# Kernel optimization log

Measured on AMD Instinct MI355X. Metric: run time of the kernel, lower is better.

Reference implementation:

```python
import jax, jax.numpy as jnp
import numpy as np

N_HEAD = 12
HEAD_SIZE = 64  # 768 / 12
SCALE = 1.0 / np.sqrt(HEAD_SIZE)


def setup_inputs() -> dict:
    key = jax.random.key(0)
    k1, k2, k3 = jax.random.split(key, 3)
    B, T, C = 8, 1024, 768
    x = jax.random.normal(k1, (B, T, C), dtype=jnp.float32)
    W_attn = jax.random.normal(k2, (C, 3 * C), dtype=jnp.float32) * 0.02
    b_attn = jax.random.normal(k3, (3 * C,), dtype=jnp.float32) * 0.02
    return {"x": x, "W_attn": W_attn, "b_attn": b_attn}


def reference(x, W_attn, b_attn):
    B, T, C = x.shape
    hs = C // N_HEAD
    qkv = x @ W_attn + b_attn                      # [B, T, 3C]
    q, k, v = jnp.split(qkv, 3, axis=-1)
    # [B, nh, T, hs]
    q = q.reshape(B, T, N_HEAD, hs).transpose(0, 2, 1, 3)
    k = k.reshape(B, T, N_HEAD, hs).transpose(0, 2, 1, 3)
    v = v.reshape(B, T, N_HEAD, hs).transpose(0, 2, 1, 3)
    scores = jnp.einsum('bhqd,bhkd->bhqk', q, k) * SCALE
    causal = jnp.tril(jnp.ones((T, T), dtype=bool))  # [T, T]
    # masked positions get -inf then relu -> 0; equivalent to where(mask, relu, 0)
    att = jnp.where(causal, jax.nn.relu(scores), 0.0)
    y = jnp.einsum('bhqk,bhkd->bhqd', att, v)      # [B, nh, T, hs]
    return y.transpose(0, 2, 1, 3).reshape(B, T, C)
```

## Files before the change

### kernel.cpp

```cpp
#include <hip/hip_runtime.h>
#include <stdint.h>

typedef __bf16 bf16;
typedef __attribute__((ext_vector_type(8))) __bf16 bf16x8;
typedef __attribute__((ext_vector_type(4))) __bf16 bf16x4;
typedef __attribute__((ext_vector_type(4))) float  f32x4;

#define ATT_SCALE 0.125f

__device__ __forceinline__ void async16(void* lds, const void* g) {
  __builtin_amdgcn_global_load_lds(
      (__attribute__((address_space(1))) void*)(void*)g,
      (__attribute__((address_space(3))) void*)lds,
      16, 0, 0);
}

__global__ void prep_kernel(const float* __restrict__ x, bf16* __restrict__ y,
                            const float* __restrict__ W, bf16* __restrict__ Wt) {
  __shared__ float tile[32][33];
  const int tid = threadIdx.x;
  if (blockIdx.x < 3072) {
    size_t i = ((size_t)blockIdx.x * 256 + tid) * 8;
    float4 a = *(const float4*)(x + i);
    float4 b = *(const float4*)(x + i + 4);
    bf16x8 o;
    o[0] = (bf16)a.x; o[1] = (bf16)a.y; o[2] = (bf16)a.z; o[3] = (bf16)a.w;
    o[4] = (bf16)b.x; o[5] = (bf16)b.y; o[6] = (bf16)b.z; o[7] = (bf16)b.w;
    *(bf16x8*)(y + i) = o;
  } else {
    const int bid = blockIdx.x - 3072;
    const int tx = tid & 31, ty = tid >> 5;
    const int n0 = (bid % 72) * 32, k0 = (bid / 72) * 32;
#pragma unroll
    for (int r = 0; r < 4; ++r)
      tile[ty + r * 8][tx] = W[(size_t)(k0 + ty + r * 8) * 2304 + n0 + tx];
    __syncthreads();
#pragma unroll
    for (int r = 0; r < 4; ++r)
      Wt[(size_t)(n0 + ty + r * 8) * 768 + k0 + tx] = (bf16)tile[tx][ty + r * 8];
  }
}

__global__ void qkv_gemm_kernel(const bf16* __restrict__ A, const bf16* __restrict__ Bw,
                                const float* __restrict__ bias,
                                bf16* __restrict__ Qo, bf16* __restrict__ Ko,
                                bf16* __restrict__ Vo) {
  __shared__ __align__(16) char lds[65536];

  const int tid  = threadIdx.x;
  const int wave = tid >> 6, lane = tid & 63;
  const int quad = lane >> 4, mn = lane & 15;
  const int wr = wave >> 1, wc = wave & 1;
  const int m0 = blockIdx.y * 128;
  const int n0 = blockIdx.x * 128;

  f32x4 acc[4][4] = {};

  const int lrow = lane >> 3;
  const int cg   = (lane & 7) ^ lrow;

  auto stage = [&](int kt, char* buf) {
    char* Al = buf;
    char* Bl = buf + 16384;
#pragma unroll
    for (int u = 0; u < 4; ++u) {
      const int t   = wave * 4 + u;
      const int row = t * 8 + lrow;
      async16(Al + t * 1024 + lane * 16,
              A  + (size_t)(m0 + row) * 768 + kt + cg * 8);
      async16(Bl + t * 1024 + lane * 16,
              Bw + (size_t)(n0 + row) * 768 + kt + cg * 8);
    }
  };

  stage(0, lds);
  int p = 0;
  for (int kt = 0; kt < 768; kt += 64) {
    __syncthreads();
    if (kt + 64 < 768) stage(kt + 64, lds + (p ^ 1) * 32768);
    char* Al = lds + p * 32768;
    char* Bl = Al + 16384;

#pragma unroll
    for (int s = 0; s < 2; ++s) {
      bf16x8 af[4], bfr[4];
      const int csw = ((s * 4 + quad) ^ (mn & 7)) * 16;
#pragma unroll
      for (int i = 0; i < 4; ++i) {
        af[i]  = *(const bf16x8*)(Al + (wr * 64 + i * 16 + mn) * 128 + csw);
        bfr[i] = *(const bf16x8*)(Bl + (wc * 64 + i * 16 + mn) * 128 + csw);
      }
#pragma unroll
      for (int i = 0; i < 4; ++i)
#pragma unroll
        for (int j = 0; j < 4; ++j)
          acc[i][j] = __builtin_amdgcn_mfma_f32_16x16x32_bf16(af[i], bfr[j], acc[i][j], 0, 0, 0);
    }
    p ^= 1;
  }

  const int ng    = n0 + wc * 64;
  const int third = ng / 768;
  const int nmod  = ng % 768;
  const float sc  = (third == 0) ? ATT_SCALE : 1.0f;
#pragma unroll
  for (int ct = 0; ct < 4; ++ct) {
    int n = nmod + ct * 16 + mn;
    int h = n >> 6, d = n & 63;
    float bv = bias[third * 768 + n];
#pragma unroll
    for (int rt = 0; rt < 4; ++rt) {
      int m  = m0 + wr * 64 + rt * 16 + quad * 4;
      int b  = m >> 10, t0 = m & 1023;
      size_t bh = (size_t)b * 12 + h;
      if (third == 2) {
        bf16x4 pk;
#pragma unroll
        for (int r = 0; r < 4; ++r) pk[r] = (bf16)(acc[rt][ct][r] + bv);
        *(bf16x4*)(Vo + (bh * 64 + d) * 1024 + t0) = pk;
      } else {
        bf16* dst = (third == 0 ? Qo : Ko) + (bh * 1024 + t0) * 64 + d;
#pragma unroll
        for (int r = 0; r < 4; ++r) dst[(size_t)r * 64] = (bf16)((acc[rt][ct][r] + bv) * sc);
      }
    }
  }
}

__global__ __launch_bounds__(256, 3)
void attn_kernel(const bf16* __restrict__ Q, const bf16* __restrict__ K,
                 const bf16* __restrict__ Vt, float* __restrict__ out) {
  __shared__ __align__(16) char lds[49152];
  char* ldsS = lds + 32768;

  const int tid  = threadIdx.x;
  const int wave = tid >> 6, lane = tid & 63;
  const int quad = lane >> 4, mn = lane & 15;
  const int bh  = blockIdx.x;
  const int qta = blockIdx.y;
  const int qtb = 15 - qta;
  const int qa0 = qta * 64, qb0 = qtb * 64;

  const bf16* Qg  = Q  + (size_t)bh * 65536;
  const bf16* Kg0 = K  + (size_t)bh * 65536;
  const bf16* Vg0 = Vt + (size_t)bh * 65536;

  bf16x8 qfA[2], qfB[2];
  {
    const bf16* ra = Qg + (size_t)(qa0 + wave * 16 + mn) * 64;
    qfA[0] = *(const bf16x8*)(ra + quad * 8);
    qfA[1] = *(const bf16x8*)(ra + 32 + quad * 8);
    const bf16* rb = Qg + (size_t)(qb0 + wave * 16 + mn) * 64;
    qfB[0] = *(const bf16x8*)(rb + quad * 8);
    qfB[1] = *(const bf16x8*)(rb + 32 + quad * 8);
  }

  f32x4 yA[4] = {}, yB[4] = {};

  const int lrow = lane >> 3;
  const int cg   = (lane & 7) ^ lrow;

  auto stageKV = [&](int j, char* buf) {
#pragma unroll
    for (int u2 = 0; u2 < 2; ++u2) {
      const int u   = wave * 2 + u2;
      const int row = u * 8 + lrow;
      async16(buf + u * 1024 + lane * 16,
              Kg0 + (size_t)(j * 64 + row) * 64 + cg * 8);
      async16(buf + 8192 + u * 1024 + lane * 16,
              Vg0 + (size_t)row * 1024 + j * 64 + cg * 8);
    }
  };

  const int srow = (wave * 16 + mn) * 128;

  stageKV(0, lds);
  for (int j = 0; j <= qtb; ++j) {
    __syncthreads();
    if (j < qtb) stageKV(j + 1, lds + ((j + 1) & 1) * 16384);
    char* bK = lds + (j & 1) * 16384;
    char* bV = bK + 8192;

    bf16x8 kf[4][2], vf[4][2];
    const int sw = mn & 7;
#pragma unroll
    for (int ct = 0; ct < 4; ++ct) {
      const int ro = (ct * 16 + mn) * 128;
      kf[ct][0] = *(const bf16x8*)(bK + ro + ((quad)     ^ sw) * 16);
      kf[ct][1] = *(const bf16x8*)(bK + ro + ((4 + quad) ^ sw) * 16);
      vf[ct][0] = *(const bf16x8*)(bV + ro + ((quad)     ^ sw) * 16);
      vf[ct][1] = *(const bf16x8*)(bV + ro + ((4 + quad) ^ sw) * 16);
    }

    auto qk_half = [&](const bf16x8* qf, int half, int qrow, bool diag) {
#pragma unroll
      for (int ct = 0; ct < 4; ++ct) {
        f32x4 a = {};
        a = __builtin_amdgcn_mfma_f32_16x16x32_bf16(kf[ct][0], qf[0], a, 0, 0, 0);
        a = __builtin_amdgcn_mfma_f32_16x16x32_bf16(kf[ct][1], qf[1], a, 0, 0, 0);
        const int kkg = j * 64 + ct * 16 + quad * 4;
        bf16x4 pk;
#pragma unroll
        for (int r = 0; r < 4; ++r) {
          float v = a[r];
          v = v > 0.f ? v : 0.f;
          if (diag && kkg + r > qrow) v = 0.f;
          pk[r] = (bf16)v;
        }
        *(bf16x4*)(ldsS + half * 8192 + srow +
                   (((ct * 4 + quad) ^ (sw << 1)) & 15) * 8) = pk;
      }
    };
    auto sv_half = [&](f32x4* y, int half) {
#pragma unroll
      for (int kb = 0; kb < 2; ++kb) {
        bf16x8 sf = *(const bf16x8*)(ldsS + half * 8192 + srow +
                                     ((kb * 4 + quad) ^ sw) * 16);
#pragma unroll
        for (int ct = 0; ct < 4; ++ct)
          y[ct] = __builtin_amdgcn_mfma_f32_16x16x32_bf16(sf, vf[ct][kb], y[ct], 0, 0, 0);
      }
    };

    if (j <= qta) qk_half(qfA, 0, qa0 + wave * 16 + mn, j == qta);
    qk_half(qfB, 1, qb0 + wave * 16 + mn, j == qtb);
    if (j <= qta) sv_half(yA, 0);
    sv_half(yB, 1);
  }

  const int b = bh / 12, h = bh % 12;
  {
    float* ob = out + ((size_t)b * 1024 + qa0 + wave * 16 + quad * 4) * 768 + h * 64;
#pragma unroll
    for (int ct = 0; ct < 4; ++ct)
#pragma unroll
      for (int r = 0; r < 4; ++r)
        ob[(size_t)r * 768 + ct * 16 + mn] = yA[ct][r];
  }
  {
    float* ob = out + ((size_t)b * 1024 + qb0 + wave * 16 + quad * 4) * 768 + h * 64;
#pragma unroll
    for (int ct = 0; ct < 4; ++ct)
#pragma unroll
      for (int r = 0; r < 4; ++r)
        ob[(size_t)r * 768 + ct * 16 + mn] = yB[ct][r];
  }
}

extern "C" void kernel_launch(void* const* d_in, const int* in_sizes, int n_in,
                              void* d_out, int out_size, void* d_ws, size_t ws_size,
                              hipStream_t stream) {
  const float* x    = (const float*)d_in[0];
  const float* W    = (const float*)d_in[1];
  const float* bias = (const float*)d_in[2];
  float* out = (float*)d_out;

  char* ws = (char*)d_ws;
  bf16* xb = (bf16*)(ws);
  bf16* Wt = (bf16*)(ws + 12582912);
  bf16* Qb = (bf16*)(ws + 16121856);
  bf16* Kb = (bf16*)(ws + 28704768);
  bf16* Vb = (bf16*)(ws + 41287680);

  prep_kernel<<<4800, 256, 0, stream>>>(x, xb, W, Wt);
  qkv_gemm_kernel<<<dim3(18, 64), 256, 0, stream>>>(xb, Wt, bias, Qb, Kb, Vb);
  attn_kernel<<<dim3(96, 8), 256, 0, stream>>>(Qb, Kb, Vb, out);
}
```

Measured before the change: 157.2 us.

## Enlarge QKV GEMM tiles to 256x256 with 8 waves and interleaved async pipeline

The QKV projection GEMM moves from 128x128 tiles with 4 waves to 256x256 tiles with 8 waves and 128KB of double-buffered LDS. Each k-step is split into four quadrant sub-steps. Half-tile async global-to-LDS loads are interleaved between them, and explicit barriers, waitcnts, sched_barriers and setprio keep MFMA work overlapped with loads. The aim is more data reuse per block and less load latency exposed to the matrix units. The cost is fewer blocks (288), higher register and LDS pressure, and a fragile hand-written schedule.

```diff
diff --git a/kernel.cpp b/kernel.cpp
--- a/kernel.cpp
+++ b/kernel.cpp
@@ -41,87 +41,147 @@
   }
 }
 
-__global__ void qkv_gemm_kernel(const bf16* __restrict__ A, const bf16* __restrict__ Bw,
-                                const float* __restrict__ bias,
-                                bf16* __restrict__ Qo, bf16* __restrict__ Ko,
-                                bf16* __restrict__ Vo) {
-  __shared__ __align__(16) char lds[65536];
+__global__ __launch_bounds__(512, 2)
+void qkv_gemm_kernel(const bf16* __restrict__ A, const bf16* __restrict__ Bw,
+                     const float* __restrict__ bias,
+                     bf16* __restrict__ Qo, bf16* __restrict__ Ko,
+                     bf16* __restrict__ Vo) {
+  __shared__ __align__(16) char lds[131072];
 
   const int tid  = threadIdx.x;
   const int wave = tid >> 6, lane = tid & 63;
   const int quad = lane >> 4, mn = lane & 15;
-  const int wr = wave >> 1, wc = wave & 1;
-  const int m0 = blockIdx.y * 128;
-  const int n0 = blockIdx.x * 128;
-
-  f32x4 acc[4][4] = {};
+  const int wr = wave >> 2, wc = wave & 3;
+  const int m0 = blockIdx.y * 256;
+  const int n0 = blockIdx.x * 256;
+
+  f32x4 acc[8][4] = {};
 
   const int lrow = lane >> 3;
   const int cg   = (lane & 7) ^ lrow;
 
-  auto stage = [&](int kt, char* buf) {
-    char* Al = buf;
-    char* Bl = buf + 16384;
-#pragma unroll
-    for (int u = 0; u < 4; ++u) {
-      const int t   = wave * 4 + u;
-      const int row = t * 8 + lrow;
-      async16(Al + t * 1024 + lane * 16,
-              A  + (size_t)(m0 + row) * 768 + kt + cg * 8);
-      async16(Bl + t * 1024 + lane * 16,
-              Bw + (size_t)(n0 + row) * 768 + kt + cg * 8);
-    }
-  };
-
-  stage(0, lds);
-  int p = 0;
-  for (int kt = 0; kt < 768; kt += 64) {
-    __syncthreads();
-    if (kt + 64 < 768) stage(kt + 64, lds + (p ^ 1) * 32768);
-    char* Al = lds + p * 32768;
-    char* Bl = Al + 16384;
-
-#pragma unroll
-    for (int s = 0; s < 2; ++s) {
-      bf16x8 af[4], bfr[4];
-      const int csw = ((s * 4 + quad) ^ (mn & 7)) * 16;
-#pragma unroll
-      for (int i = 0; i < 4; ++i) {
-        af[i]  = *(const bf16x8*)(Al + (wr * 64 + i * 16 + mn) * 128 + csw);
-        bfr[i] = *(const bf16x8*)(Bl + (wc * 64 + i * 16 + mn) * 128 + csw);
-      }
-#pragma unroll
-      for (int i = 0; i < 4; ++i)
-#pragma unroll
-        for (int j = 0; j < 4; ++j)
-          acc[i][j] = __builtin_amdgcn_mfma_f32_16x16x32_bf16(af[i], bfr[j], acc[i][j], 0, 0, 0);
-    }
-    p ^= 1;
-  }
+  auto stageH = [&](int t, int op, int half) {
+    char* dst = lds + (t & 1) * 65536 + op * 32768 + half * 16384;
+    const bf16* src = op ? Bw : A;
+    const int  r0   = (op ? n0 : m0) + half * 128;
+#pragma unroll
+    for (int u = 0; u < 2; ++u) {
+      const int grp = wave * 2 + u;
+      const int row = grp * 8 + lrow;
+      async16(dst + grp * 1024 + lane * 16,
+              src + (size_t)(r0 + row) * 768 + t * 64 + cg * 8);
+    }
+  };
+
+  bf16x8 af[4][2], bf0[2][2], bf1[2][2];
+  auto ldA = [&](int t, int a) {
+    const char* base = lds + (t & 1) * 65536 + wr * 16384;
+#pragma unroll
+    for (int i = 0; i < 4; ++i) {
+      const int r = a * 64 + i * 16 + mn;
+#pragma unroll
+      for (int s = 0; s < 2; ++s)
+        af[i][s] = *(const bf16x8*)(base + r * 128 + (((s * 4 + quad) ^ (mn & 7)) * 16));
+    }
+  };
+  auto ldB = [&](int t, int b, bf16x8 (&bfr)[2][2]) {
+    const char* base = lds + (t & 1) * 65536 + 32768 + (wc >> 1) * 16384;
+#pragma unroll
+    for (int j = 0; j < 2; ++j) {
+      const int r = (wc & 1) * 64 + b * 32 + j * 16 + mn;
+#pragma unroll
+      for (int s = 0; s < 2; ++s)
+        bfr[j][s] = *(const bf16x8*)(base + r * 128 + (((s * 4 + quad) ^ (mn & 7)) * 16));
+    }
+  };
+  auto mm = [&](bf16x8 (&bfr)[2][2], int a, int b) {
+    __builtin_amdgcn_s_setprio(1);
+#pragma unroll
+    for (int i = 0; i < 4; ++i)
+#pragma unroll
+      for (int j = 0; j < 2; ++j)
+#pragma unroll
+        for (int s = 0; s < 2; ++s)
+          acc[a * 4 + i][b * 2 + j] = __builtin_amdgcn_mfma_f32_16x16x32_bf16(
+              af[i][s], bfr[j][s], acc[a * 4 + i][b * 2 + j], 0, 0, 0);
+    __builtin_amdgcn_s_setprio(0);
+  };
+
+#define SCHED0() __builtin_amdgcn_sched_barrier(0)
+#define BAR()    do { __builtin_amdgcn_s_barrier(); SCHED0(); } while (0)
+#define LGKM0()  do { asm volatile("s_waitcnt lgkmcnt(0)" ::: "memory"); SCHED0(); } while (0)
+#define VM4()    do { asm volatile("s_waitcnt vmcnt(4)" ::: "memory"); SCHED0(); } while (0)
+#define VM0()    do { asm volatile("s_waitcnt vmcnt(0)" ::: "memory"); SCHED0(); } while (0)
+
+  stageH(0, 1, 0); SCHED0();
+  stageH(0, 0, 0); SCHED0();
+  stageH(0, 1, 1); SCHED0();
+  stageH(0, 0, 1); SCHED0();
+  stageH(1, 1, 0); SCHED0();
+  stageH(1, 0, 0); SCHED0();
+  VM0();
+  BAR();
+
+  for (int P = 0; P < 6; ++P) {
+    const int t0 = 2 * P, t1 = 2 * P + 1;
+    const bool s2 = (t0 + 2) < 12, s3 = (t0 + 3) < 12;
+
+    ldA(t0, 0); ldB(t0, 0, bf0);
+    stageH(t1, 1, 1); SCHED0();
+    BAR(); LGKM0(); mm(bf0, 0, 0); BAR();
+    ldB(t0, 1, bf1);
+    stageH(t1, 0, 1); SCHED0();
+    BAR(); LGKM0(); mm(bf1, 0, 1); BAR();
+    ldA(t0, 1);
+    if (s2) { stageH(t0 + 2, 1, 0); SCHED0(); }
+    BAR(); LGKM0(); mm(bf1, 1, 1); BAR();
+    if (s2) { stageH(t0 + 2, 0, 0); SCHED0(); }
+    if (P == 5) { VM0(); } else { VM4(); }
+    BAR(); mm(bf0, 1, 0); BAR();
+
+    ldA(t1, 0); ldB(t1, 0, bf0);
+    if (s2) { stageH(t0 + 2, 1, 1); SCHED0(); }
+    BAR(); LGKM0(); mm(bf0, 0, 0); BAR();
+    ldB(t1, 1, bf1);
+    if (s2) { stageH(t0 + 2, 0, 1); SCHED0(); }
+    BAR(); LGKM0(); mm(bf1, 0, 1); BAR();
+    ldA(t1, 1);
+    if (s3) { stageH(t0 + 3, 1, 0); SCHED0(); }
+    BAR(); LGKM0(); mm(bf1, 1, 1); BAR();
+    if (s3) { stageH(t0 + 3, 0, 0); SCHED0(); }
+    VM4();
+    BAR(); mm(bf0, 1, 0); BAR();
+  }
+
+#undef BAR
+#undef LGKM0
+#undef VM4
+#undef VM0
+#undef SCHED0
 
   const int ng    = n0 + wc * 64;
   const int third = ng / 768;
   const int nmod  = ng % 768;
   const float sc  = (third == 0) ? ATT_SCALE : 1.0f;
 #pragma unroll
-  for (int ct = 0; ct < 4; ++ct) {
-    int n = nmod + ct * 16 + mn;
+  for (int bj = 0; bj < 4; ++bj) {
+    int n = nmod + bj * 16 + mn;
     int h = n >> 6, d = n & 63;
     float bv = bias[third * 768 + n];
 #pragma unroll
-    for (int rt = 0; rt < 4; ++rt) {
-      int m  = m0 + wr * 64 + rt * 16 + quad * 4;
-      int b  = m >> 10, t0 = m & 1023;
+    for (int ai = 0; ai < 8; ++ai) {
+      int m  = m0 + wr * 128 + ai * 16 + quad * 4;
+      int b  = m >> 10, t0r = m & 1023;
       size_t bh = (size_t)b * 12 + h;
       if (third == 2) {
         bf16x4 pk;
 #pragma unroll
-        for (int r = 0; r < 4; ++r) pk[r] = (bf16)(acc[rt][ct][r] + bv);
-        *(bf16x4*)(Vo + (bh * 64 + d) * 1024 + t0) = pk;
+        for (int r = 0; r < 4; ++r) pk[r] = (bf16)(acc[ai][bj][r] + bv);
+        *(bf16x4*)(Vo + (bh * 64 + d) * 1024 + t0r) = pk;
       } else {
-        bf16* dst = (third == 0 ? Qo : Ko) + (bh * 1024 + t0) * 64 + d;
-#pragma unroll
-        for (int r = 0; r < 4; ++r) dst[(size_t)r * 64] = (bf16)((acc[rt][ct][r] + bv) * sc);
+        bf16* dst = (third == 0 ? Qo : Ko) + (bh * 1024 + t0r) * 64 + d;
+#pragma unroll
+        for (int r = 0; r < 4; ++r) dst[(size_t)r * 64] = (bf16)((acc[ai][bj][r] + bv) * sc);
       }
     }
   }
@@ -263,6 +323,6 @@
   bf16* Vb = (bf16*)(ws + 41287680);
 
   prep_kernel<<<4800, 256, 0, stream>>>(x, xb, W, Wt);
-  qkv_gemm_kernel<<<dim3(18, 64), 256, 0, stream>>>(xb, Wt, bias, Qb, Kb, Vb);
+  qkv_gemm_kernel<<<dim3(9, 32), 512, 0, stream>>>(xb, Wt, bias, Qb, Kb, Vb);
   attn_kernel<<<dim3(96, 8), 256, 0, stream>>>(Qb, Kb, Vb, out);
 }
```

Result: no change. 156.2 us (-0.6%).
